# Kernel optimization log

Hardware: AMD Instinct MI355X
Metric: run time of the kernel (lower is better)

Reference implementation:

```python
import jax, jax.numpy as jnp
import numpy as np

NUM_RBF = 64
CUTOFF = 5.0
N_GRAPHS = 64


def _rbf_expand(d):
    # Gaussian RBF expansion on [0, CUTOFF] with cosine cutoff envelope.
    mus = jnp.linspace(0.0, CUTOFF, NUM_RBF, dtype=d.dtype)  # [M]
    gamma = (NUM_RBF / CUTOFF) ** 2  # 1 / spacing^2
    fc = 0.5 * (jnp.cos(jnp.pi * d / CUTOFF) + 1.0) * (d < CUTOFF)  # [E]
    return jnp.exp(-gamma * (d[:, None] - mus[None, :]) ** 2) * fc[:, None]  # [E,M]


def setup_inputs() -> dict:
    key = jax.random.key(0)
    k0, k1, k2, k3, k4, k5 = jax.random.split(key, 6)
    N, E, T = 50000, 1600000, 25
    pos = jax.random.normal(k0, (N, 3), jnp.float32) * 3.0
    edge_index = jax.random.randint(k1, (2, E), 0, N)
    atom_types = jax.random.randint(k2, (N,), 0, T)
    batch = jnp.sort(jax.random.randint(k3, (N,), 0, N_GRAPHS))
    rbf_params = jax.random.normal(k4, (T, T, NUM_RBF), jnp.float32)
    radial_filters = jax.random.uniform(k5, (T, T, NUM_RBF), jnp.float32)
    return {
        "pos": pos,
        "rbf_params": rbf_params,
        "radial_filters": radial_filters,
        "edge_index": edge_index,
        "atom_types": atom_types,
        "batch": batch,
    }


def reference(pos, rbf_params, radial_filters, edge_index, atom_types, batch):
    src, dst = edge_index[0], edge_index[1]
    # distances (no cell shifts)
    diff = pos[dst] - pos[src]                       # [E,3]
    d = jnp.sqrt(jnp.sum(diff * diff, axis=-1) + 1e-12)  # [E]
    # type-pair lookup with canonical ordering (sender <= receiver)
    s = atom_types[src]
    r = atom_types[dst]
    lo = jnp.minimum(s, r)
    hi = jnp.maximum(s, r)
    params = rbf_params[lo, hi]        # [E,M]
    filt = radial_filters[lo, hi]      # [E,M] (already in [0,1])
    expn = _rbf_expand(d) * filt       # filtered RBF expansion
    e_edge = jnp.sum(expn * params, axis=1)  # [E]
    # reduce per-edge energies to per-graph energies
    bmap = batch[src]
    energy = jax.ops.segment_sum(e_edge, bmap, num_segments=N_GRAPHS)  # [G]
    return energy
```

## Files before the change

### kernel.cpp

```cpp
#include <hip/hip_runtime.h>
#include <math.h>

#define NUM_RBF 64
#define N_GRAPHS 64

typedef int   int4v   __attribute__((ext_vector_type(4)));
typedef float float4v __attribute__((ext_vector_type(4)));


__global__ __launch_bounds__(256) void prologue_kernel(
    const float4v* __restrict__ p, const float4v* __restrict__ f,
    float4v* __restrict__ C, int n4,
    const float* __restrict__ pos, const int* __restrict__ types,
    const int* __restrict__ batch, float4v* __restrict__ rec, int N)
{
    int i = blockIdx.x * blockDim.x + threadIdx.x;
    if (i < n4) C[i] = p[i] * f[i];
    if (i < N) {
        int bits = (types[i] & 0xFF) | ((batch[i] & 0xFF) << 8);
        float4v r = { pos[3 * i], pos[3 * i + 1], pos[3 * i + 2],
                      __int_as_float(bits) };
        rec[i] = r;
    }
}

#define CUTOFF2_F     25.0f
#define GAMMA_F       163.84f
#define SPACING_F     (float)(5.0 / 63.0)
#define INV_SPACING_F (float)(63.0 / 5.0)
#define PI_OVER_C_F   (float)(3.14159265358979323846 / 5.0)
#define TWO_GAMMA_S_F (float)(2.0 * 163.84 * 5.0 / 63.0)
#define LN_V          (-(64.0 / 63.0) * (64.0 / 63.0))
#define V_1           (float)exp(LN_V)
#define V_2           (float)exp(2.0 * LN_V)

__device__ __forceinline__ void edge_body(
    float4v rs, float4v rd, const float4v* __restrict__ C4, int T,
    float* __restrict__ bins)
{
    const float dx = rd.x - rs.x;
    const float dy = rd.y - rs.y;
    const float dz = rd.z - rs.z;
    const float d2 = dx * dx + dy * dy + dz * dz + 1e-12f;
    if (d2 >= CUTOFF2_F) return;

    const float d = sqrtf(d2);
    const int sb = __float_as_int(rs.w);
    const int ts = sb & 0xFF;
    const int td = __float_as_int(rd.w) & 0xFF;
    const int lo = min(ts, td);
    const int hi = max(ts, td);
    const int base = (lo * T + hi) * NUM_RBF;

    const float c = d * INV_SPACING_F;
    int a0 = ((int)floorf(c - 1.5f)) & ~3;
    a0 = max(0, min(NUM_RBF - 8, a0));

    const float4v* w = C4 + ((base + a0) >> 2);
    const float4v w0 = w[0], w1 = w[1];

    const float delta = d - (float)a0 * SPACING_F;
    float t = __expf(-GAMMA_F * delta * delta);
    const float u = __expf(TWO_GAMMA_S_F * delta);
    float m = u * V_1;

    float acc = w0.x * t;
    t *= m;  m *= V_2;  acc += w0.y * t;
    t *= m;  m *= V_2;  acc += w0.z * t;
    t *= m;  m *= V_2;  acc += w0.w * t;
    t *= m;  m *= V_2;  acc += w1.x * t;
    t *= m;  m *= V_2;  acc += w1.y * t;
    t *= m;  m *= V_2;  acc += w1.z * t;
    t *= m;            acc += w1.w * t;

    const float fc = 0.5f * (__cosf(PI_OVER_C_F * d) + 1.0f);
    atomicAdd(&bins[(sb >> 8) & 0xFF], acc * fc);
}

__global__ __launch_bounds__(256) void edge_energy_kernel(
    const int*     __restrict__ edge_index,
    const float4v* __restrict__ rec,
    const float4v* __restrict__ C4,
    float*         __restrict__ partial,
    int E, int T)
{
    __shared__ float bins[N_GRAPHS];
    const int tid = threadIdx.x;
    for (int i = tid; i < N_GRAPHS; i += blockDim.x) bins[i] = 0.0f;
    __syncthreads();

    const int nfull  = E >> 2;
    const int stride = gridDim.x * blockDim.x;
    const int gid    = blockIdx.x * blockDim.x + tid;

    for (int q = gid; q < nfull; q += stride) {
        const int e0 = q << 2;
        const int4v sv = __builtin_nontemporal_load(
            (const int4v*)(edge_index + e0));
        const int4v tv = __builtin_nontemporal_load(
            (const int4v*)(edge_index + E + e0));

        const float4v rs0 = rec[sv.x], rd0 = rec[tv.x];
        const float4v rs1 = rec[sv.y], rd1 = rec[tv.y];
        const float4v rs2 = rec[sv.z], rd2 = rec[tv.z];
        const float4v rs3 = rec[sv.w], rd3 = rec[tv.w];

        edge_body(rs0, rd0, C4, T, bins);
        edge_body(rs1, rd1, C4, T, bins);
        edge_body(rs2, rd2, C4, T, bins);
        edge_body(rs3, rd3, C4, T, bins);
    }

    if (gid == 0) {
        for (int e = nfull << 2; e < E; ++e) {
            const float4v rs = rec[edge_index[e]];
            const float4v rd = rec[edge_index[E + e]];
            edge_body(rs, rd, C4, T, bins);
        }
    }

    __syncthreads();
    for (int i = tid; i < N_GRAPHS; i += blockDim.x)
        partial[blockIdx.x * N_GRAPHS + i] = bins[i];
}

__global__ __launch_bounds__(256) void reduce_kernel(
    const float* __restrict__ partial, float* __restrict__ out, int nblocks)
{
    const int g = blockIdx.x;
    float s = 0.0f;
    for (int i = threadIdx.x; i < nblocks; i += blockDim.x)
        s += partial[i * N_GRAPHS + g];

    for (int off = 32; off > 0; off >>= 1)
        s += __shfl_down(s, off, 64);

    __shared__ float red[4];
    const int wave = threadIdx.x >> 6;
    const int lane = threadIdx.x & 63;
    if (lane == 0) red[wave] = s;
    __syncthreads();
    if (threadIdx.x == 0)
        out[g] = red[0] + red[1] + red[2] + red[3];
}

extern "C" void kernel_launch(void* const* d_in, const int* in_sizes, int n_in,
                              void* d_out, int out_size, void* d_ws, size_t ws_size,
                              hipStream_t stream) {
    const float* pos            = (const float*)d_in[0];
    const float* rbf_params     = (const float*)d_in[1];
    const float* radial_filters = (const float*)d_in[2];
    const int*   edge_index     = (const int*)d_in[3];
    const int*   atom_types     = (const int*)d_in[4];
    const int*   batch          = (const int*)d_in[5];
    float*       out            = (float*)d_out;

    const int E = in_sizes[3] / 2;
    const int N = in_sizes[4];
    int T = 1;
    while ((T + 1) * (T + 1) * NUM_RBF <= in_sizes[1]) ++T;
    const int tbl_elems = T * T * NUM_RBF;

    float*   Ctab    = (float*)d_ws;
    float4v* recs    = (float4v*)((char*)d_ws + ((size_t)tbl_elems * 4 + 255) / 256 * 256);
    float*   partial = (float*)((char*)recs + (size_t)N * 16);

    const int nq = E >> 2;
    int nblocks = (nq + 255) / 256;
    const size_t part_off = (size_t)((char*)partial - (char*)d_ws);
    const size_t avail = (ws_size > part_off) ? (ws_size - part_off) : 0;
    const int maxb = (int)(avail / (N_GRAPHS * sizeof(float)));
    if (nblocks > maxb) nblocks = maxb > 0 ? maxb : 1;
    if (nblocks < 1) nblocks = 1;

    const int pro_n = max(tbl_elems / 4, N);
    prologue_kernel<<<(pro_n + 255) / 256, 256, 0, stream>>>(
        (const float4v*)rbf_params, (const float4v*)radial_filters,
        (float4v*)Ctab, tbl_elems / 4, pos, atom_types, batch, recs, N);
    edge_energy_kernel<<<nblocks, 256, 0, stream>>>(
        edge_index, recs, (const float4v*)Ctab, partial, E, T);
    reduce_kernel<<<N_GRAPHS, 256, 0, stream>>>(partial, out, nblocks);
}
```

Baseline: 94.99 us.

## Store premultiplied RBF table in fp16 and widen Gaussian window to sixteen basis functions

The premultiplied params*filter table is now stored as half precision, which halves its footprint and lets each edge fetch 16 coefficients in two 16-byte loads. The RBF window grows from 8 to 16 terms around the distance, computed outward from the center with forward and inverse exponential recurrences. This improves truncation accuracy and reduces cache pressure on table gathers. In exchange it adds an exp, more FMAs and fp16 conversions per edge, and introduces fp16 rounding of the weights.

```diff
diff --git a/kernel.cpp b/kernel.cpp
--- a/kernel.cpp
+++ b/kernel.cpp
@@ -4,18 +4,24 @@
 #define NUM_RBF 64
 #define N_GRAPHS 64
 
-typedef int   int4v   __attribute__((ext_vector_type(4)));
-typedef float float4v __attribute__((ext_vector_type(4)));
+typedef int      int4v   __attribute__((ext_vector_type(4)));
+typedef float    float4v __attribute__((ext_vector_type(4)));
+typedef _Float16 h4      __attribute__((ext_vector_type(4)));
+typedef _Float16 h8      __attribute__((ext_vector_type(8)));
 
 
 __global__ __launch_bounds__(256) void prologue_kernel(
     const float4v* __restrict__ p, const float4v* __restrict__ f,
-    float4v* __restrict__ C, int n4,
+    h4* __restrict__ Ch, int n4,
     const float* __restrict__ pos, const int* __restrict__ types,
     const int* __restrict__ batch, float4v* __restrict__ rec, int N)
 {
     int i = blockIdx.x * blockDim.x + threadIdx.x;
-    if (i < n4) C[i] = p[i] * f[i];
+    if (i < n4) {
+        float4v a = p[i] * f[i];
+        h4 hv = { (_Float16)a.x, (_Float16)a.y, (_Float16)a.z, (_Float16)a.w };
+        Ch[i] = hv;
+    }
     if (i < N) {
         int bits = (types[i] & 0xFF) | ((batch[i] & 0xFF) << 8);
         float4v r = { pos[3 * i], pos[3 * i + 1], pos[3 * i + 2],
@@ -35,7 +41,7 @@
 #define V_2           (float)exp(2.0 * LN_V)
 
 __device__ __forceinline__ void edge_body(
-    float4v rs, float4v rd, const float4v* __restrict__ C4, int T,
+    float4v rs, float4v rd, const _Float16* __restrict__ Ch, int T,
     float* __restrict__ bins)
 {
     const float dx = rd.x - rs.x;
@@ -53,35 +59,47 @@
     const int base = (lo * T + hi) * NUM_RBF;
 
     const float c = d * INV_SPACING_F;
-    int a0 = ((int)floorf(c - 1.5f)) & ~3;
-    a0 = max(0, min(NUM_RBF - 8, a0));
-
-    const float4v* w = C4 + ((base + a0) >> 2);
-    const float4v w0 = w[0], w1 = w[1];
+    int a0 = ((int)floorf(c - 3.5f)) & ~7;
+    a0 = max(0, min(NUM_RBF - 16, a0));
+
+    const h8* w = (const h8*)(Ch + base + a0);
+    const h8 wa = w[0], wb = w[1];
 
     const float delta = d - (float)a0 * SPACING_F;
-    float t = __expf(-GAMMA_F * delta * delta);
-    const float u = __expf(TWO_GAMMA_S_F * delta);
-    float m = u * V_1;
-
-    float acc = w0.x * t;
-    t *= m;  m *= V_2;  acc += w0.y * t;
-    t *= m;  m *= V_2;  acc += w0.z * t;
-    t *= m;  m *= V_2;  acc += w0.w * t;
-    t *= m;  m *= V_2;  acc += w1.x * t;
-    t *= m;  m *= V_2;  acc += w1.y * t;
-    t *= m;  m *= V_2;  acc += w1.z * t;
-    t *= m;            acc += w1.w * t;
+    const float d7 = delta - 7.0f * SPACING_F;
+    const float t7 = __expf(-GAMMA_F * d7 * d7);
+    const float x  = TWO_GAMMA_S_F * d7;
+    const float u  = __expf(x);
+    const float ui = __expf(-x);
+
+    float acc = (float)wa[7] * t7;
+    float t = t7, m = u * V_1;
+    t *= m;  acc += (float)wb[0] * t;  m *= V_2;
+    t *= m;  acc += (float)wb[1] * t;  m *= V_2;
+    t *= m;  acc += (float)wb[2] * t;  m *= V_2;
+    t *= m;  acc += (float)wb[3] * t;  m *= V_2;
+    t *= m;  acc += (float)wb[4] * t;  m *= V_2;
+    t *= m;  acc += (float)wb[5] * t;  m *= V_2;
+    t *= m;  acc += (float)wb[6] * t;  m *= V_2;
+    t *= m;  acc += (float)wb[7] * t;
+    t = t7;  m = ui * V_1;
+    t *= m;  acc += (float)wa[6] * t;  m *= V_2;
+    t *= m;  acc += (float)wa[5] * t;  m *= V_2;
+    t *= m;  acc += (float)wa[4] * t;  m *= V_2;
+    t *= m;  acc += (float)wa[3] * t;  m *= V_2;
+    t *= m;  acc += (float)wa[2] * t;  m *= V_2;
+    t *= m;  acc += (float)wa[1] * t;  m *= V_2;
+    t *= m;  acc += (float)wa[0] * t;
 
     const float fc = 0.5f * (__cosf(PI_OVER_C_F * d) + 1.0f);
     atomicAdd(&bins[(sb >> 8) & 0xFF], acc * fc);
 }
 
 __global__ __launch_bounds__(256) void edge_energy_kernel(
-    const int*     __restrict__ edge_index,
-    const float4v* __restrict__ rec,
-    const float4v* __restrict__ C4,
-    float*         __restrict__ partial,
+    const int*      __restrict__ edge_index,
+    const float4v*  __restrict__ rec,
+    const _Float16* __restrict__ Ch,
+    float*          __restrict__ partial,
     int E, int T)
 {
     __shared__ float bins[N_GRAPHS];
@@ -105,17 +123,17 @@
         const float4v rs2 = rec[sv.z], rd2 = rec[tv.z];
         const float4v rs3 = rec[sv.w], rd3 = rec[tv.w];
 
-        edge_body(rs0, rd0, C4, T, bins);
-        edge_body(rs1, rd1, C4, T, bins);
-        edge_body(rs2, rd2, C4, T, bins);
-        edge_body(rs3, rd3, C4, T, bins);
+        edge_body(rs0, rd0, Ch, T, bins);
+        edge_body(rs1, rd1, Ch, T, bins);
+        edge_body(rs2, rd2, Ch, T, bins);
+        edge_body(rs3, rd3, Ch, T, bins);
     }
 
     if (gid == 0) {
         for (int e = nfull << 2; e < E; ++e) {
             const float4v rs = rec[edge_index[e]];
             const float4v rd = rec[edge_index[E + e]];
-            edge_body(rs, rd, C4, T, bins);
+            edge_body(rs, rd, Ch, T, bins);
         }
     }
 
@@ -161,9 +179,9 @@
     while ((T + 1) * (T + 1) * NUM_RBF <= in_sizes[1]) ++T;
     const int tbl_elems = T * T * NUM_RBF;
 
-    float*   Ctab    = (float*)d_ws;
-    float4v* recs    = (float4v*)((char*)d_ws + ((size_t)tbl_elems * 4 + 255) / 256 * 256);
-    float*   partial = (float*)((char*)recs + (size_t)N * 16);
+    _Float16* Ch     = (_Float16*)d_ws;
+    float4v*  recs   = (float4v*)((char*)d_ws + ((size_t)tbl_elems * 2 + 255) / 256 * 256);
+    float*    partial = (float*)((char*)recs + (size_t)N * 16);
 
     const int nq = E >> 2;
     int nblocks = (nq + 255) / 256;
@@ -176,8 +194,8 @@
     const int pro_n = max(tbl_elems / 4, N);
     prologue_kernel<<<(pro_n + 255) / 256, 256, 0, stream>>>(
         (const float4v*)rbf_params, (const float4v*)radial_filters,
-        (float4v*)Ctab, tbl_elems / 4, pos, atom_types, batch, recs, N);
+        (h4*)Ch, tbl_elems / 4, pos, atom_types, batch, recs, N);
     edge_energy_kernel<<<nblocks, 256, 0, stream>>>(
-        edge_index, recs, (const float4v*)Ctab, partial, E, T);
+        edge_index, recs, Ch, partial, E, T);
     reduce_kernel<<<N_GRAPHS, 256, 0, stream>>>(partial, out, nblocks);
 }
```

New measurement: 96.05 us. No clear change (+1.1%).
